# Performance work log

Measured on AMD Instinct MI355X. Metric: run time of the kernel, lower is better.

The kernel has to match this reference:

```python
import jax, jax.numpy as jnp
import numpy as np

N_HEADS = 8


def _norm_weights(idx):
    # softmax over where(idx>0, 1, -9e15) along axis 1 -> uniform weights over non-pad slots
    logits = jnp.where(idx > 0, jnp.float32(1.0), jnp.float32(-9e15))
    return jax.nn.softmax(logits, axis=1)


def _layer_norm(x, g, b, eps=1e-6):
    mu = jnp.mean(x, axis=-1, keepdims=True)
    var = jnp.var(x, axis=-1, keepdims=True)
    return (x - mu) * jax.lax.rsqrt(var + eps) * g + b


def _mha_block(x, mask, wq, wk, wv, wo, g, b):
    # standard multi-head self-attention block with residual + layernorm
    B, L, D = x.shape
    hd = D // N_HEADS
    q = (x @ wq).reshape(B, L, N_HEADS, hd)
    k = (x @ wk).reshape(B, L, N_HEADS, hd)
    v = (x @ wv).reshape(B, L, N_HEADS, hd)
    scores = jnp.einsum('bqhd,bkhd->bhqk', q, k) / jnp.float32(np.sqrt(hd))
    scores = jnp.where(mask[:, None, None, :], jnp.float32(-1e9), scores)
    attn = jax.nn.softmax(scores, axis=-1)
    out = jnp.einsum('bhqk,bkhd->bqhd', attn, v).reshape(B, L, D) @ wo
    return _layer_norm(out + x, g, b)


def _forward(data_idx, seq, timestamps, user_level, useq, user_inf, user_cen,
             spread_status, id2vector,
             user_emb, cen_emb, time_emb, pos_emb, inf_emb,
             w1, w2, w3,
             t_wq, t_wk, t_wv, t_wo, t_g, t_b,
             s_wq, s_wk, s_wv, s_wo, s_g, s_b,
             W, W2, f_l1_w, f_l1_b, f_l2_w, f_l2_b, lin_w, lin_b):
    # ---- HGNN layer (hypergraph conv) ----
    tv = w3[0]  # TextVector = weight3[0]
    dot = w3 @ tv
    cos = dot / (jnp.linalg.norm(tv) * jnp.linalg.norm(w3, axis=1))
    inter_nw = jnp.mean(cos)  # scalar

    tweet_hidden = user_emb + cen_emb[user_cen]          # [N, D]
    x = (tweet_hidden @ w1) * inter_nw                   # [N, D]
    nor = _norm_weights(seq)                             # [E, L]
    edge = jnp.einsum('elc,el->ec', x[seq], nor)         # gather + weighted reduce
    edge = jax.nn.relu(edge)
    e1 = edge @ w2                                       # [E, D]
    u_nor = _norm_weights(useq)                          # [N, Lu]
    node = jnp.einsum('nlc,nl->nc', e1[useq], u_nor)     # [N, D]

    # ---- HGSL head ----
    sb = seq[data_idx]                                   # [B, L]
    nor_b = _norm_weights(sb)
    att_mask = sb == 0                                   # PAD == 0
    adj = node[sb]                                       # [B, L, D]

    att_hidden = adj + time_emb[timestamps[data_idx]]
    att_out = _mha_block(att_hidden, att_mask, t_wq, t_wk, t_wv, t_wo, t_g, t_b)
    news = jnp.einsum('blc,bl->bc', att_out, nor_b)
    news = jnp.concatenate([news, spread_status[data_idx][:, 2:] / 3600.0 / 24.0], axis=-1) @ W

    att_hidden_s = adj + inf_emb[user_inf[data_idx]] + pos_emb[user_level[data_idx]]
    att_out_s = _mha_block(att_hidden_s, att_mask, s_wq, s_wk, s_wv, s_wo, s_g, s_b)
    news_s = jnp.einsum('blc,bl->bc', att_out_s, nor_b)
    news_s = jnp.concatenate([news_s, spread_status[data_idx][:, :2]], axis=-1) @ W2

    # Gated fusion (linear3 unused in original forward; id2vector is overwritten/unused)
    emb = jnp.stack([news, news_s], axis=0)              # [2, B, D+2]
    score = jax.nn.softmax(jnp.tanh(emb @ f_l1_w + f_l1_b) @ f_l2_w + f_l2_b, axis=0)
    fused = jnp.sum(score * emb, axis=0)                 # [B, D+2]
    return jax.nn.log_softmax(fused @ lin_w + lin_b, axis=1)


def setup_inputs():
    key = jax.random.key(0)
    ks = jax.random.split(key, 40)
    N, E, L, Lu, D, B, TV = 50000, 10000, 50, 20, 128, 512, 768
    Dw = D + 2
    s = 0.05
    inp = {
        'data_idx': jax.random.randint(ks[0], (B,), 0, E),
        'seq': jax.random.randint(ks[1], (E, L), 0, N),
        'timestamps': jax.random.randint(ks[2], (E, L), 0, 5000),
        'user_level': jax.random.randint(ks[3], (E, L), 0, 50),
        'useq': jax.random.randint(ks[4], (N, Lu), 0, E),
        'user_inf': jax.random.randint(ks[5], (E, L), 0, 200),
        'user_cen': jax.random.randint(ks[6], (N,), 0, 600),
        'spread_status': jax.random.uniform(ks[7], (E, 4), dtype=jnp.float32),
        'id2vector': jax.random.normal(ks[8], (1,), dtype=jnp.float32),
        'user_emb': s * jax.random.normal(ks[9], (N, D), dtype=jnp.float32),
        'cen_emb': s * jax.random.normal(ks[10], (600, D), dtype=jnp.float32),
        'time_emb': s * jax.random.normal(ks[11], (5000, D), dtype=jnp.float32),
        'pos_emb': s * jax.random.normal(ks[12], (50, D), dtype=jnp.float32),
        'inf_emb': s * jax.random.normal(ks[13], (200, D), dtype=jnp.float32),
        'w1': s * jax.random.normal(ks[14], (D, D), dtype=jnp.float32),
        'w2': s * jax.random.normal(ks[15], (D, D), dtype=jnp.float32),
        'w3': s * jax.random.normal(ks[16], (TV, TV), dtype=jnp.float32),
        'W': s * jax.random.normal(ks[17], (Dw, Dw), dtype=jnp.float32),
        'W2': s * jax.random.normal(ks[18], (Dw, Dw), dtype=jnp.float32),
        'f_l1_w': s * jax.random.normal(ks[19], (Dw, Dw), dtype=jnp.float32),
        'f_l1_b': jnp.zeros((Dw,), jnp.float32),
        'f_l2_w': s * jax.random.normal(ks[20], (Dw, 1), dtype=jnp.float32),
        'f_l2_b': jnp.zeros((1,), jnp.float32),
        'lin_w': s * jax.random.normal(ks[21], (Dw, 2), dtype=jnp.float32),
        'lin_b': jnp.zeros((2,), jnp.float32),
    }
    for nm, i in [('t', 22), ('s', 27)]:
        inp[nm + '_wq'] = s * jax.random.normal(ks[i], (D, D), dtype=jnp.float32)
        inp[nm + '_wk'] = s * jax.random.normal(ks[i + 1], (D, D), dtype=jnp.float32)
        inp[nm + '_wv'] = s * jax.random.normal(ks[i + 2], (D, D), dtype=jnp.float32)
        inp[nm + '_wo'] = s * jax.random.normal(ks[i + 3], (D, D), dtype=jnp.float32)
        inp[nm + '_g'] = jnp.ones((D,), jnp.float32)
        inp[nm + '_b'] = jnp.zeros((D,), jnp.float32)
    return inp


def reference(data_idx, seq, timestamps, user_level, useq, user_inf, user_cen,
              spread_status, id2vector,
              user_emb, cen_emb, time_emb, pos_emb, inf_emb,
              w1, w2, w3,
              t_wq, t_wk, t_wv, t_wo, t_g, t_b,
              s_wq, s_wk, s_wv, s_wo, s_g, s_b,
              W, W2, f_l1_w, f_l1_b, f_l2_w, f_l2_b, lin_w, lin_b):
    return _forward(data_idx, seq, timestamps, user_level, useq, user_inf, user_cen,
                    spread_status, id2vector,
                    user_emb, cen_emb, time_emb, pos_emb, inf_emb,
                    w1, w2, w3,
                    t_wq, t_wk, t_wv, t_wo, t_g, t_b,
                    s_wq, s_wk, s_wv, s_wo, s_g, s_b,
                    W, W2, f_l1_w, f_l1_b, f_l2_w, f_l2_b, lin_w, lin_b)
```

## Files before the change

### kernel.cpp

```cpp
#include <hip/hip_runtime.h>
#include <math.h>

constexpr int Nn = 50000;
constexpr int Ee = 10000;
constexpr int Ll = 50;
constexpr int LuU = 20;
constexpr int Dd = 128;
constexpr int Bb = 512;
constexpr int TVv = 768;
constexpr int Dw = 130;
constexpr int BL = Bb * Ll;

typedef __attribute__((ext_vector_type(8))) short bf8v;
typedef __attribute__((ext_vector_type(4))) float f4v;
typedef __attribute__((ext_vector_type(8))) unsigned short u16x8;
typedef __attribute__((ext_vector_type(4))) unsigned short u16x4;

__device__ __forceinline__ unsigned short f2bf(float f) {
  union { float f; unsigned u; } v; v.f = f;
  unsigned r = v.u + 0x7FFFu + ((v.u >> 16) & 1u);
  return (unsigned short)(r >> 16);
}
__device__ __forceinline__ float bf2f(unsigned short h) {
  union { unsigned u; float f; } v; v.u = ((unsigned)h) << 16; return v.f;
}
__device__ __forceinline__ int swz(int b) { return b ^ (((b >> 8) & 7) << 4); }
__device__ __forceinline__ int swzp(int b) { return b ^ (((b >> 7) & 3) << 4); }

__device__ __forceinline__ float block_sum_256(float v, volatile float* scr) {
#pragma unroll
  for (int o = 32; o > 0; o >>= 1) v += __shfl_down(v, o, 64);
  __syncthreads();
  if ((threadIdx.x & 63) == 0) scr[threadIdx.x >> 6] = v;
  __syncthreads();
  return scr[0] + scr[1] + scr[2] + scr[3];
}

__global__ __launch_bounds__(256) void k_cos(const float* __restrict__ w3,
                                             float* __restrict__ dotb,
                                             float* __restrict__ nrmb) {
  __shared__ float scr[4];
  int i = blockIdx.x;
  const float* row = w3 + (size_t)i * TVv;
  float d = 0.f, n = 0.f;
  for (int j = threadIdx.x; j < TVv; j += 256) {
    float a = row[j];
    d += a * w3[j];
    n += a * a;
  }
  d = block_sum_256(d, scr);
  n = block_sum_256(n, scr);
  if (threadIdx.x == 0) { dotb[i] = d; nrmb[i] = n; }
}

__global__ __launch_bounds__(256) void k_internw(const float* __restrict__ dotb,
                                                 const float* __restrict__ nrmb,
                                                 float* __restrict__ internw) {
  __shared__ float scr[4];
  float n0 = sqrtf(nrmb[0]);
  float s = 0.f;
  for (int i = threadIdx.x; i < TVv; i += 256)
    s += dotb[i] / (n0 * sqrtf(nrmb[i]));
  s = block_sum_256(s, scr);
  if (threadIdx.x == 0) *internw = s / (float)TVv;
}

__global__ __launch_bounds__(256) void k_prep(
    const float* w1, const float* w2,
    const float* twq, const float* twk, const float* twv, const float* two,
    const float* swq, const float* swk, const float* swv, const float* swo,
    unsigned short* __restrict__ out) {
  int wsel = blockIdx.x >> 3, part = blockIdx.x & 7;
  const float* w;
  switch (wsel) {
    case 0: w = w1; break;  case 1: w = w2; break;
    case 2: w = twq; break; case 3: w = twk; break;
    case 4: w = twv; break; case 5: w = two; break;
    case 6: w = swq; break; case 7: w = swk; break;
    case 8: w = swv; break; default: w = swo; break;
  }
  int u = part * 256 + threadIdx.x;
  int n = u >> 4, k0 = (u & 15) * 8;
  u16x8 pv;
#pragma unroll
  for (int i = 0; i < 8; i++) pv[i] = f2bf(w[(size_t)(k0 + i) * Dd + n]);
  ((u16x8*)(out + (size_t)wsel * Dd * Dd))[u] = pv;
}

template <int MODE>
__global__ __launch_bounds__(256) void k_gemm_plain(
    const void* __restrict__ inA, const float* __restrict__ in1,
    const int* __restrict__ gidx, const float* __restrict__ scalep,
    const unsigned short* __restrict__ WTg,
    unsigned short* __restrict__ out, int nrows) {
  __shared__ unsigned short WT[Dd * Dd];
  __shared__ __align__(16) unsigned short Ab[64 * Dd];
  int tid = threadIdx.x;
  {
    const u16x8* src = (const u16x8*)WTg;
    for (int u = tid; u < 2048; u += 256)
      *(u16x8*)((char*)WT + swz(u * 16)) = src[u];
  }
  int r0 = blockIdx.x * 64;
  if constexpr (MODE == 0) {
    float sc = *scalep;
    for (int u = tid; u < 1024; u += 256) {
      int rr = u >> 4, c0 = (u & 15) * 8;
      int r = r0 + rr;
      u16x8 pv;
      if (r < nrows) {
        const float* a = (const float*)inA + (size_t)r * Dd + c0;
        const float* c = in1 + (size_t)gidx[r] * Dd + c0;
#pragma unroll
        for (int i = 0; i < 8; i++) pv[i] = f2bf((a[i] + c[i]) * sc);
      } else {
#pragma unroll
        for (int i = 0; i < 8; i++) pv[i] = 0;
      }
      *(u16x8*)((char*)Ab + swz(rr * 256 + c0 * 2)) = pv;
    }
  } else {
    for (int u = tid; u < 1024; u += 256) {
      int rr = u >> 4;
      int r = r0 + rr;
      u16x8 pv;
      if (r < nrows) pv = ((const u16x8*)inA)[(size_t)r * 16 + (u & 15)];
      else {
#pragma unroll
        for (int i = 0; i < 8; i++) pv[i] = 0;
      }
      *(u16x8*)((char*)Ab + swz(rr * 256 + (u & 15) * 16)) = pv;
    }
  }
  __syncthreads();
  int lane = tid & 63, wid = tid >> 6;
  int lrow = lane & 15, lg = lane >> 4;
  bf8v af[4];
#pragma unroll
  for (int kc = 0; kc < 4; kc++)
    af[kc] = *(const bf8v*)((char*)Ab + swz((wid * 16 + lrow) * 256 + kc * 64 + lg * 16));
  f4v acc[8];
#pragma unroll
  for (int nt = 0; nt < 8; nt++)
#pragma unroll
    for (int j = 0; j < 4; j++) acc[nt][j] = 0.f;
#pragma unroll
  for (int nt = 0; nt < 8; nt++)
#pragma unroll
    for (int kc = 0; kc < 4; kc++) {
      bf8v bfg = *(const bf8v*)((char*)WT + swz((nt * 16 + lrow) * 256 + kc * 64 + lg * 16));
      acc[nt] = __builtin_amdgcn_mfma_f32_16x16x32_bf16(af[kc], bfg, acc[nt], 0, 0, 0);
    }
#pragma unroll
  for (int nt = 0; nt < 8; nt++)
#pragma unroll
    for (int j = 0; j < 4; j++) {
      int r = r0 + wid * 16 + lg * 4 + j;
      if (r < nrows) out[(size_t)r * Dd + nt * 16 + lrow] = f2bf(acc[nt][j]);
    }
}

__global__ __launch_bounds__(256) void k_gemm_qkv(
    const unsigned short* __restrict__ hidT, const unsigned short* __restrict__ hidS,
    const unsigned short* __restrict__ WTbase,
    unsigned short* __restrict__ outQ, unsigned short* __restrict__ outK,
    unsigned short* __restrict__ outV) {
  __shared__ unsigned short WT[Dd * Dd];
  __shared__ __align__(16) unsigned short Ab[128 * Dd];
  int tile = blockIdx.x % 200, branch = blockIdx.x / 200;
  const unsigned short* in = branch ? hidS : hidT;
  int r0 = tile * 128;
  int tid = threadIdx.x;
  for (int u = tid; u < 2048; u += 256) {
    int rr = u >> 4, ch = u & 15;
    u16x8 pv = ((const u16x8*)in)[(size_t)(r0 + rr) * 16 + ch];
    *(u16x8*)((char*)Ab + swz(rr * 256 + ch * 16)) = pv;
  }
  {
    const u16x8* srcW = (const u16x8*)(WTbase + (size_t)(2 + branch * 4) * Dd * Dd);
    for (int u = tid; u < 2048; u += 256)
      *(u16x8*)((char*)WT + swz(u * 16)) = srcW[u];
  }
  __syncthreads();
  int lane = tid & 63, wid = tid >> 6;
  int lrow = lane & 15, lg = lane >> 4;
  bf8v af[2][4];
#pragma unroll
  for (int mi = 0; mi < 2; mi++)
#pragma unroll
    for (int kc = 0; kc < 4; kc++)
      af[mi][kc] = *(const bf8v*)((char*)Ab +
                    swz((wid * 32 + mi * 16 + lrow) * 256 + kc * 64 + lg * 16));
#pragma unroll 1
  for (int sel = 0; sel < 3; sel++) {
    f4v acc[2][8];
#pragma unroll
    for (int mi = 0; mi < 2; mi++)
#pragma unroll
      for (int nt = 0; nt < 8; nt++)
#pragma unroll
        for (int j = 0; j < 4; j++) acc[mi][nt][j] = 0.f;
#pragma unroll
    for (int nt = 0; nt < 8; nt++)
#pragma unroll
      for (int kc = 0; kc < 4; kc++) {
        bf8v bfg = *(const bf8v*)((char*)WT + swz((nt * 16 + lrow) * 256 + kc * 64 + lg * 16));
        acc[0][nt] = __builtin_amdgcn_mfma_f32_16x16x32_bf16(af[0][kc], bfg, acc[0][nt], 0, 0, 0);
        acc[1][nt] = __builtin_amdgcn_mfma_f32_16x16x32_bf16(af[1][kc], bfg, acc[1][nt], 0, 0, 0);
      }
    unsigned short* outb = ((sel == 0) ? outQ : (sel == 1) ? outK : outV)
                           + (size_t)branch * BL * Dd;
#pragma unroll
    for (int mi = 0; mi < 2; mi++)
#pragma unroll
      for (int nt = 0; nt < 8; nt++)
#pragma unroll
        for (int j = 0; j < 4; j++) {
          int r = r0 + wid * 32 + mi * 16 + lg * 4 + j;
          outb[(size_t)r * Dd + nt * 16 + lrow] = f2bf(acc[mi][nt][j]);
        }
    if (sel < 2) {
      __syncthreads();
      const u16x8* srcW = (const u16x8*)(WTbase + (size_t)(2 + branch * 4 + sel + 1) * Dd * Dd);
      for (int u = tid; u < 2048; u += 256)
        *(u16x8*)((char*)WT + swz(u * 16)) = srcW[u];
      __syncthreads();
    }
  }
}

__global__ __launch_bounds__(256) void k_gemm_ln(
    const unsigned short* __restrict__ ctxall,
    const unsigned short* __restrict__ hidT, const unsigned short* __restrict__ hidS,
    const unsigned short* __restrict__ WTbase,
    const float* __restrict__ tg, const float* __restrict__ tb,
    const float* __restrict__ sg, const float* __restrict__ sb_,
    unsigned short* __restrict__ attall) {
  __shared__ unsigned short WT[Dd * Dd];
  __shared__ __align__(16) char UB[64 * 132 * 4];
  unsigned short* Ab = (unsigned short*)UB;
  float (*O)[132] = (float (*)[132])UB;

  int tile = blockIdx.x % 400, branch = blockIdx.x / 400;
  const unsigned short* in = ctxall + (size_t)branch * BL * Dd;
  const unsigned short* resid = (branch ? hidS : hidT);
  const unsigned short* Wg = WTbase + (size_t)(5 + branch * 4) * Dd * Dd;
  const float* lng = branch ? sg : tg;
  const float* lnb = branch ? sb_ : tb;
  unsigned short* out = attall + (size_t)branch * BL * Dd;
  int r0 = tile * 64;
  int tid = threadIdx.x;

  {
    const u16x8* src = (const u16x8*)Wg;
    for (int u = tid; u < 2048; u += 256)
      *(u16x8*)((char*)WT + swz(u * 16)) = src[u];
  }
  for (int u = tid; u < 1024; u += 256) {
    int rr = u >> 4;
    u16x8 pv = ((const u16x8*)in)[(size_t)(r0 + rr) * 16 + (u & 15)];
    *(u16x8*)((char*)Ab + swz(rr * 256 + (u & 15) * 16)) = pv;
  }
  __syncthreads();

  int lane = tid & 63, wid = tid >> 6;
  int lrow = lane & 15, lg = lane >> 4;
  bf8v af[4];
#pragma unroll
  for (int kc = 0; kc < 4; kc++)
    af[kc] = *(const bf8v*)((char*)Ab + swz((wid * 16 + lrow) * 256 + kc * 64 + lg * 16));
  f4v acc[8];
#pragma unroll
  for (int nt = 0; nt < 8; nt++)
#pragma unroll
    for (int j = 0; j < 4; j++) acc[nt][j] = 0.f;
#pragma unroll
  for (int nt = 0; nt < 8; nt++)
#pragma unroll
    for (int kc = 0; kc < 4; kc++) {
      bf8v bfg = *(const bf8v*)((char*)WT + swz((nt * 16 + lrow) * 256 + kc * 64 + lg * 16));
      acc[nt] = __builtin_amdgcn_mfma_f32_16x16x32_bf16(af[kc], bfg, acc[nt], 0, 0, 0);
    }
  __syncthreads();
#pragma unroll
  for (int nt = 0; nt < 8; nt++)
#pragma unroll
    for (int j = 0; j < 4; j++)
      O[wid * 16 + lg * 4 + j][nt * 16 + lrow] = acc[nt][j];
  __syncthreads();
  int r = tid >> 2, c0 = (tid & 3) * 32;
  size_t gr = (size_t)(r0 + r);
  float vv[32];
  float s1 = 0.f, s2 = 0.f;
#pragma unroll
  for (int i8 = 0; i8 < 4; i8++) {
    u16x8 hb = *(const u16x8*)(resid + gr * Dd + c0 + i8 * 8);
#pragma unroll
    for (int i = 0; i < 8; i++) {
      float x = O[r][c0 + i8 * 8 + i] + bf2f(hb[i]);
      vv[i8 * 8 + i] = x; s1 += x; s2 += x * x;
    }
  }
  s1 += __shfl_xor(s1, 1, 64); s2 += __shfl_xor(s2, 1, 64);
  s1 += __shfl_xor(s1, 2, 64); s2 += __shfl_xor(s2, 2, 64);
  float mu = s1 * (1.f / Dd);
  float var = s2 * (1.f / Dd) - mu * mu;
  float rs = rsqrtf(var + 1e-6f);
#pragma unroll
  for (int i8 = 0; i8 < 4; i8++) {
    u16x8 ov;
#pragma unroll
    for (int i = 0; i < 8; i++) {
      int c = c0 + i8 * 8 + i;
      ov[i] = f2bf((vv[i8 * 8 + i] - mu) * rs * lng[c] + lnb[c]);
    }
    *(u16x8*)(out + gr * Dd + c0 + i8 * 8) = ov;
  }
}

__global__ __launch_bounds__(256) void k_gather_e(const unsigned short* __restrict__ X,
                                                  const int* __restrict__ seq,
                                                  unsigned short* __restrict__ EDGE) {
  int r = blockIdx.x * 16 + (threadIdx.x >> 4);
  int c0 = (threadIdx.x & 15) * 8;
  const int* row = seq + (size_t)r * Ll;
  float acc[8];
#pragma unroll
  for (int i = 0; i < 8; i++) acc[i] = 0.f;
  int cnt = 0;
#pragma unroll 1
  for (int l0 = 0; l0 < Ll; l0 += 10) {
    int ids[10];
#pragma unroll
    for (int t = 0; t < 10; t++) ids[t] = row[l0 + t];
    u16x8 vv[10];
#pragma unroll
    for (int t = 0; t < 10; t++)
      vv[t] = *(const u16x8*)(X + (size_t)ids[t] * Dd + c0);
#pragma unroll
    for (int t = 0; t < 10; t++)
      if (ids[t] > 0) {
        cnt++;
#pragma unroll
        for (int i = 0; i < 8; i++) acc[i] += bf2f(vv[t][i]);
      }
  }
  u16x8 ov;
  if (cnt) {
    float inv = 1.f / (float)cnt;
#pragma unroll
    for (int i = 0; i < 8; i++) ov[i] = f2bf(fmaxf(acc[i] * inv, 0.f));
  } else {
    u16x8 x0 = *(const u16x8*)(X + c0);
#pragma unroll
    for (int i = 0; i < 8; i++) ov[i] = f2bf(fmaxf(bf2f(x0[i]), 0.f));
  }
  *(u16x8*)(EDGE + (size_t)r * Dd + c0) = ov;
}

__global__ __launch_bounds__(256) void k_hidfuse(
    const unsigned short* __restrict__ E1, const int* __restrict__ data_idx,
    const int* __restrict__ seq, const int* __restrict__ tsmp,
    const int* __restrict__ uinf, const int* __restrict__ ulev,
    const int* __restrict__ useq,
    const float* __restrict__ time_emb, const float* __restrict__ inf_emb,
    const float* __restrict__ pos_emb,
    unsigned short* __restrict__ hidTb, unsigned short* __restrict__ hidSb) {
  int bl = blockIdx.x * 16 + (threadIdx.x >> 4);
  int c0 = (threadIdx.x & 15) * 8;
  int b = bl / Ll, l = bl % Ll;
  int e = data_idx[b];
  int sid = seq[(size_t)e * Ll + l];
  const int* urow = useq + (size_t)sid * LuU;
  float acc[8];
#pragma unroll
  for (int i = 0; i < 8; i++) acc[i] = 0.f;
  int cnt = 0;
#pragma unroll 1
  for (int t0 = 0; t0 < LuU; t0 += 10) {
    int ids[10];
#pragma unroll
    for (int t = 0; t < 10; t++) ids[t] = urow[t0 + t];
    u16x8 vv[10];
#pragma unroll
    for (int t = 0; t < 10; t++)
      vv[t] = *(const u16x8*)(E1 + (size_t)ids[t] * Dd + c0);
#pragma unroll
    for (int t = 0; t < 10; t++)
      if (ids[t] > 0) {
        cnt++;
#pragma unroll
        for (int i = 0; i < 8; i++) acc[i] += bf2f(vv[t][i]);
      }
  }
  float node[8];
  if (cnt) {
    float inv = 1.f / (float)cnt;
#pragma unroll
    for (int i = 0; i < 8; i++) node[i] = acc[i] * inv;
  } else {
    u16x8 e0 = *(const u16x8*)(E1 + c0);
#pragma unroll
    for (int i = 0; i < 8; i++) node[i] = bf2f(e0[i]);
  }
  int ts = tsmp[(size_t)e * Ll + l];
  int fi = uinf[(size_t)e * Ll + l];
  int lv = ulev[(size_t)e * Ll + l];
  const float4* tp = (const float4*)(time_emb + (size_t)ts * Dd + c0);
  const float4* ip = (const float4*)(inf_emb + (size_t)fi * Dd + c0);
  const float4* pp = (const float4*)(pos_emb + (size_t)lv * Dd + c0);
  float4 t0 = tp[0], t1 = tp[1];
  float4 i0 = ip[0], i1 = ip[1];
  float4 p0 = pp[0], p1 = pp[1];
  float te[8] = {t0.x, t0.y, t0.z, t0.w, t1.x, t1.y, t1.z, t1.w};
  float ie[8] = {i0.x, i0.y, i0.z, i0.w, i1.x, i1.y, i1.z, i1.w};
  float pe[8] = {p0.x, p0.y, p0.z, p0.w, p1.x, p1.y, p1.z, p1.w};
  u16x8 ht, hs;
#pragma unroll
  for (int i = 0; i < 8; i++) {
    ht[i] = f2bf(node[i] + te[i]);
    hs[i] = f2bf(node[i] + ie[i] + pe[i]);
  }
  size_t o = (size_t)bl * Dd + c0;
  *(u16x8*)(hidTb + o) = ht;
  *(u16x8*)(hidSb + o) = hs;
}

__global__ __launch_bounds__(256) void k_attn_mfma(
    const unsigned short* __restrict__ qall,
    const unsigned short* __restrict__ kall,
    const unsigned short* __restrict__ vall,
    const int* __restrict__ data_idx,
    const int* __restrict__ seq,
    unsigned short* __restrict__ ctxall) {
  __shared__ __align__(16) unsigned short QKV[3 * 64 * 128];
  __shared__ __align__(16) unsigned short PT[4 * 64 * 64];
  __shared__ int maskl[Ll];
  int b = blockIdx.x, branch = blockIdx.y;
  size_t boff = (size_t)branch * BL * Dd + (size_t)b * Ll * Dd;
  const unsigned short* qg = qall + boff;
  const unsigned short* kg = kall + boff;
  const unsigned short* vg = vall + boff;
  int tid = threadIdx.x;
  int e = data_idx[b];
  if (tid < Ll) maskl[tid] = (seq[(size_t)e * Ll + tid] == 0);
  for (int u = tid; u < 3072; u += 256) {
    int t = u >> 10, rem = u & 1023;
    int row = rem >> 4, ch = rem & 15;
    u16x8 pv;
    if (row < Ll) {
      const unsigned short* src = (t == 0) ? qg : (t == 1) ? kg : vg;
      pv = *(const u16x8*)(src + (size_t)row * Dd + ch * 8);
    } else {
#pragma unroll
      for (int i = 0; i < 8; i++) pv[i] = 0;
    }
    *(u16x8*)((char*)QKV + t * 16384 + swz(row * 256 + ch * 16)) = pv;
  }
  __syncthreads();
  int lane = tid & 63, wid = tid >> 6;
  int lrow = lane & 15, lg = lane >> 4;
  const char* Qb = (const char*)QKV;
  const char* Kb = (const char*)QKV + 16384;
  const char* Vb = (const char*)QKV + 32768;
  char* PTw = (char*)PT + wid * 8192;
  unsigned short* ctx = ctxall + boff;

#pragma unroll 1
  for (int hi = 0; hi < 2; hi++) {
    int h = wid * 2 + hi;
    int cb = h * 32;
    bf8v af[4], bf[4];
    if (lg < 2) {
#pragma unroll
      for (int mt = 0; mt < 4; mt++)
        af[mt] = *(const bf8v*)(Kb + swz((mt * 16 + lrow) * 256 + cb + lg * 16));
#pragma unroll
      for (int nt = 0; nt < 4; nt++)
        bf[nt] = *(const bf8v*)(Qb + swz((nt * 16 + lrow) * 256 + cb + lg * 16));
    } else {
#pragma unroll
      for (int t = 0; t < 4; t++)
#pragma unroll
        for (int i = 0; i < 8; i++) { af[t][i] = 0; bf[t][i] = 0; }
    }
    f4v acc[16];
#pragma unroll
    for (int t = 0; t < 16; t++)
#pragma unroll
      for (int j = 0; j < 4; j++) acc[t][j] = 0.f;
#pragma unroll
    for (int mt = 0; mt < 4; mt++)
#pragma unroll
      for (int nt = 0; nt < 4; nt++)
        acc[mt * 4 + nt] =
            __builtin_amdgcn_mfma_f32_16x16x32_bf16(af[mt], bf[nt], acc[mt * 4 + nt], 0, 0, 0);
#pragma unroll
    for (int mt = 0; mt < 4; mt++)
#pragma unroll
      for (int j = 0; j < 4; j++) {
        int kk = mt * 16 + lg * 4 + j;
        bool pad = (kk >= Ll);
        bool mk = !pad && (maskl[pad ? 0 : kk] != 0);
#pragma unroll
        for (int nt = 0; nt < 4; nt++) {
          float v = acc[mt * 4 + nt][j] * 0.25f;
          v = mk ? -1e9f : v;
          v = pad ? -3.0e38f : v;
          acc[mt * 4 + nt][j] = v;
        }
      }
#pragma unroll
    for (int nt = 0; nt < 4; nt++) {
      float m = -3.0e38f;
#pragma unroll
      for (int mt = 0; mt < 4; mt++)
#pragma unroll
        for (int j = 0; j < 4; j++) m = fmaxf(m, acc[mt * 4 + nt][j]);
      m = fmaxf(m, __shfl_xor(m, 16, 64));
      m = fmaxf(m, __shfl_xor(m, 32, 64));
      float s = 0.f;
#pragma unroll
      for (int mt = 0; mt < 4; mt++)
#pragma unroll
        for (int j = 0; j < 4; j++) {
          float p = expf(acc[mt * 4 + nt][j] - m);
          acc[mt * 4 + nt][j] = p;
          s += p;
        }
      s += __shfl_xor(s, 16, 64);
      s += __shfl_xor(s, 32, 64);
      float inv = 1.f / s;
      int q = nt * 16 + lrow;
#pragma unroll
      for (int mt = 0; mt < 4; mt++) {
        u16x4 pw;
#pragma unroll
        for (int j = 0; j < 4; j++) pw[j] = f2bf(acc[mt * 4 + nt][j] * inv);
        *(u16x4*)(PTw + swzp(q * 128 + mt * 32 + lg * 8)) = pw;
      }
    }
    f4v pacc[4];
#pragma unroll
    for (int nt = 0; nt < 4; nt++)
#pragma unroll
      for (int j = 0; j < 4; j++) pacc[nt][j] = 0.f;
#pragma unroll
    for (int kt = 0; kt < 2; kt++) {
      bf8v av;
#pragma unroll
      for (int i = 0; i < 8; i++)
        av[i] = *(const short*)(Vb + swz((kt * 32 + lg * 8 + i) * 256 + cb + lrow * 2));
#pragma unroll
      for (int nt = 0; nt < 4; nt++) {
        bf8v bv = *(const bf8v*)(PTw + swzp((nt * 16 + lrow) * 128 + kt * 64 + lg * 16));
        pacc[nt] = __builtin_amdgcn_mfma_f32_16x16x32_bf16(av, bv, pacc[nt], 0, 0, 0);
      }
    }
#pragma unroll
    for (int nt = 0; nt < 4; nt++) {
      int q = nt * 16 + lrow;
      if (q < Ll) {
        u16x4 ow;
#pragma unroll
        for (int j = 0; j < 4; j++) ow[j] = f2bf(pacc[nt][j]);
        *(u16x4*)(ctx + (size_t)q * Dd + h * 16 + lg * 4) = ow;
      }
    }
  }
}

__global__ __launch_bounds__(128) void k_newsred(const unsigned short* __restrict__ attall,
                                                 const int* __restrict__ data_idx,
                                                 const int* __restrict__ seq,
                                                 const float* __restrict__ spread,
                                                 float* __restrict__ news) {
  __shared__ int sl[Ll];
  __shared__ int scnt;
  int b = blockIdx.x, branch = blockIdx.y;
  int e = data_idx[b];
  const unsigned short* att = attall + (size_t)branch * BL * Dd;
  if (threadIdx.x < Ll) sl[threadIdx.x] = seq[(size_t)e * Ll + threadIdx.x];
  __syncthreads();
  if (threadIdx.x == 0) {
    int c = 0;
    for (int l = 0; l < Ll; l++) c += (sl[l] > 0);
    scnt = c;
  }
  __syncthreads();
  int cnt = scnt;
  float wnp = cnt ? 1.f / (float)cnt : 0.02f;
  int c = threadIdx.x;
  float acc = 0.f;
  for (int l = 0; l < Ll; l++) {
    float w = cnt ? ((sl[l] > 0) ? wnp : 0.f) : wnp;
    acc += w * bf2f(att[((size_t)b * Ll + l) * Dd + c]);
  }
  float* nrow = news + ((size_t)branch * Bb + b) * 132;
  nrow[c] = acc;
  if (c < 2) {
    nrow[Dd + c] = branch ? spread[(size_t)e * 4 + c]
                          : spread[(size_t)e * 4 + 2 + c] * (1.f / 86400.f);
  }
}

__global__ __launch_bounds__(256) void k_newsW(const float* __restrict__ news,
                                               const float* __restrict__ Wm,
                                               const float* __restrict__ W2m,
                                               float* __restrict__ NT,
                                               float* __restrict__ NS) {
  __shared__ float Wl[Dw][Dw + 1];
  __shared__ float nrow[132];
  int branch = blockIdx.y;
  const float* W = branch ? W2m : Wm;
  float* out = branch ? NS : NT;
  for (int u = threadIdx.x; u < Dw * Dw; u += 256)
    Wl[u / Dw][u % Dw] = W[u];
  for (int rr = 0; rr < 32; rr++) {
    int b = blockIdx.x * 32 + rr;
    __syncthreads();
    if (threadIdx.x < Dw)
      nrow[threadIdx.x] = news[((size_t)branch * Bb + b) * 132 + threadIdx.x];
    __syncthreads();
    int j = threadIdx.x;
    if (j < Dw) {
      float acc = 0.f;
      for (int kk = 0; kk < Dw; kk++) acc += nrow[kk] * Wl[kk][j];
      out[(size_t)b * Dw + j] = acc;
    }
  }
}

__global__ __launch_bounds__(256) void k_fusion(const float* __restrict__ nt,
                                                const float* __restrict__ ns,
                                                const float* __restrict__ l1w,
                                                const float* __restrict__ l1b,
                                                const float* __restrict__ l2w,
                                                const float* __restrict__ l2b,
                                                const float* __restrict__ linw,
                                                const float* __restrict__ linb,
                                                float* __restrict__ out) {
  __shared__ float rt[Dw], rs[Dw];
  __shared__ float scr[4];
  int b = blockIdx.x, j = threadIdx.x;
  if (j < Dw) { rt[j] = nt[(size_t)b * Dw + j]; rs[j] = ns[(size_t)b * Dw + j]; }
  __syncthreads();
  float pt = 0.f, ps = 0.f;
  if (j < Dw) {
    float at = l1b[j], as = l1b[j];
    for (int kk = 0; kk < Dw; kk++) {
      float w = l1w[(size_t)kk * Dw + j];
      at += rt[kk] * w;
      as += rs[kk] * w;
    }
    float lw2 = l2w[j];
    pt = tanhf(at) * lw2;
    ps = tanhf(as) * lw2;
  }
  float st = block_sum_256(pt, scr);
  float ss = block_sum_256(ps, scr);
  st += l2b[0]; ss += l2b[0];
  float m = fmaxf(st, ss);
  float e0 = expf(st - m), e1v = expf(ss - m);
  float inv = 1.f / (e0 + e1v);
  float s0 = e0 * inv, s1 = e1v * inv;
  float fj  = (j < Dw) ? (s0 * rt[j] + s1 * rs[j]) : 0.f;
  float w0  = (j < Dw) ? linw[(size_t)j * 2 + 0] : 0.f;
  float w1v = (j < Dw) ? linw[(size_t)j * 2 + 1] : 0.f;
  float l0 = block_sum_256(fj * w0, scr);
  float l1 = block_sum_256(fj * w1v, scr);
  if (j == 0) {
    l0 += linb[0]; l1 += linb[1];
    float mm = fmaxf(l0, l1);
    float lse = mm + logf(expf(l0 - mm) + expf(l1 - mm));
    out[(size_t)b * 2 + 0] = l0 - lse;
    out[(size_t)b * 2 + 1] = l1 - lse;
  }
}

extern "C" void kernel_launch(void* const* d_in, const int* in_sizes, int n_in,
                              void* d_out, int out_size, void* d_ws, size_t ws_size,
                              hipStream_t stream) {
  const int*   data_idx = (const int*)d_in[0];
  const int*   seq      = (const int*)d_in[1];
  const int*   tsmp     = (const int*)d_in[2];
  const int*   ulev     = (const int*)d_in[3];
  const int*   useq     = (const int*)d_in[4];
  const int*   uinf     = (const int*)d_in[5];
  const int*   ucen     = (const int*)d_in[6];
  const float* spread   = (const float*)d_in[7];
  const float* user_emb = (const float*)d_in[9];
  const float* cen_emb  = (const float*)d_in[10];
  const float* time_emb = (const float*)d_in[11];
  const float* pos_emb  = (const float*)d_in[12];
  const float* inf_emb  = (const float*)d_in[13];
  const float* w1       = (const float*)d_in[14];
  const float* w2       = (const float*)d_in[15];
  const float* w3       = (const float*)d_in[16];
  const float* Wm       = (const float*)d_in[17];
  const float* W2m      = (const float*)d_in[18];
  const float* f_l1_w   = (const float*)d_in[19];
  const float* f_l1_b   = (const float*)d_in[20];
  const float* f_l2_w   = (const float*)d_in[21];
  const float* f_l2_b   = (const float*)d_in[22];
  const float* lin_w    = (const float*)d_in[23];
  const float* lin_b    = (const float*)d_in[24];
  const float* t_wq = (const float*)d_in[25];
  const float* t_wk = (const float*)d_in[26];
  const float* t_wv = (const float*)d_in[27];
  const float* t_wo = (const float*)d_in[28];
  const float* t_g  = (const float*)d_in[29];
  const float* t_b  = (const float*)d_in[30];
  const float* s_wq = (const float*)d_in[31];
  const float* s_wk = (const float*)d_in[32];
  const float* s_wv = (const float*)d_in[33];
  const float* s_wo = (const float*)d_in[34];
  const float* s_g  = (const float*)d_in[35];
  const float* s_b  = (const float*)d_in[36];

  char* ws = (char*)d_ws;
  constexpr size_t SZ_WT  = (size_t)10 * Dd * Dd * 2;
  constexpr size_t SZ_XB  = (size_t)Nn * Dd * 2;
  constexpr size_t SZ_EB  = (size_t)Ee * Dd * 2;
  constexpr size_t SZ_BH  = (size_t)BL * Dd * 2;
  constexpr size_t OFF_WT  = 8192;
  constexpr size_t OFF_X   = OFF_WT + SZ_WT;
  constexpr size_t OFF_EDGE= OFF_X + SZ_XB;
  constexpr size_t OFF_E1  = OFF_EDGE + SZ_EB;
  constexpr size_t OFF_HTB = OFF_E1 + SZ_EB;
  constexpr size_t OFF_HSB = OFF_HTB + SZ_BH;
  constexpr size_t OFF_Q   = OFF_HSB + SZ_BH;
  constexpr size_t OFF_K   = OFF_Q + 2 * SZ_BH;
  constexpr size_t OFF_V   = OFF_K + 2 * SZ_BH;
  constexpr size_t OFF_CTX = OFF_V + 2 * SZ_BH;
  constexpr size_t OFF_ATT = OFF_CTX + 2 * SZ_BH;
  constexpr size_t OFF_NEWS= OFF_ATT + 2 * SZ_BH;
  constexpr size_t OFF_NT  = OFF_NEWS + (size_t)2 * Bb * 132 * 4;
  constexpr size_t OFF_NS  = OFF_NT + (size_t)Bb * Dw * 4;

  float* dotb    = (float*)(ws + 0);
  float* nrmb    = (float*)(ws + 3072);
  float* internw = (float*)(ws + 6144);
  unsigned short* WTall = (unsigned short*)(ws + OFF_WT);
  unsigned short* Xb    = (unsigned short*)(ws + OFF_X);
  unsigned short* EDGEb = (unsigned short*)(ws + OFF_EDGE);
  unsigned short* E1b   = (unsigned short*)(ws + OFF_E1);
  unsigned short* HIDTb = (unsigned short*)(ws + OFF_HTB);
  unsigned short* HIDSb = (unsigned short*)(ws + OFF_HSB);
  unsigned short* Qall  = (unsigned short*)(ws + OFF_Q);
  unsigned short* Kall  = (unsigned short*)(ws + OFF_K);
  unsigned short* Vall  = (unsigned short*)(ws + OFF_V);
  unsigned short* CTXall= (unsigned short*)(ws + OFF_CTX);
  unsigned short* ATTall= (unsigned short*)(ws + OFF_ATT);
  float*          NEWS  = (float*)(ws + OFF_NEWS);
  float*          NT    = (float*)(ws + OFF_NT);
  float*          NS    = (float*)(ws + OFF_NS);
  float* outp = (float*)d_out;

  k_prep<<<80, 256, 0, stream>>>(w1, w2, t_wq, t_wk, t_wv, t_wo,
                                 s_wq, s_wk, s_wv, s_wo, WTall);
  k_cos<<<TVv, 256, 0, stream>>>(w3, dotb, nrmb);
  k_internw<<<1, 256, 0, stream>>>(dotb, nrmb, internw);

  k_gemm_plain<0><<<(Nn + 63) / 64, 256, 0, stream>>>(
      user_emb, cen_emb, ucen, internw, WTall + 0 * Dd * Dd, Xb, Nn);
  k_gather_e<<<Ee / 16, 256, 0, stream>>>(Xb, seq, EDGEb);
  k_gemm_plain<1><<<(Ee + 63) / 64, 256, 0, stream>>>(
      EDGEb, nullptr, nullptr, nullptr, WTall + 1 * Dd * Dd, E1b, Ee);
  k_hidfuse<<<BL / 16, 256, 0, stream>>>(E1b, data_idx, seq, tsmp, uinf, ulev, useq,
                                         time_emb, inf_emb, pos_emb, HIDTb, HIDSb);

  k_gemm_qkv<<<400, 256, 0, stream>>>(HIDTb, HIDSb, WTall, Qall, Kall, Vall);
  k_attn_mfma<<<dim3(Bb, 2), 256, 0, stream>>>(Qall, Kall, Vall, data_idx, seq, CTXall);
  k_gemm_ln<<<400 * 2, 256, 0, stream>>>(CTXall, HIDTb, HIDSb, WTall,
                                         t_g, t_b, s_g, s_b, ATTall);

  k_newsred<<<dim3(Bb, 2), 128, 0, stream>>>(ATTall, data_idx, seq, spread, NEWS);
  k_newsW<<<dim3(16, 2), 256, 0, stream>>>(NEWS, Wm, W2m, NT, NS);
  k_fusion<<<Bb, 256, 0, stream>>>(NT, NS, f_l1_w, f_l1_b, f_l2_w, f_l2_b,
                                   lin_w, lin_b, outp);

  (void)in_sizes; (void)n_in; (void)out_size; (void)ws_size;
}
```

Baseline: 357.9 us.

## Pad QKV/ctx to 64 rows per batch and store V transposed for attention

```diff
diff --git a/kernel.cpp b/kernel.cpp
--- a/kernel.cpp
+++ b/kernel.cpp
@@ -10,6 +10,7 @@
 constexpr int TVv = 768;
 constexpr int Dw = 130;
 constexpr int BL = Bb * Ll;
+constexpr int BLP = Bb * 64;
 
 typedef __attribute__((ext_vector_type(8))) short bf8v;
 typedef __attribute__((ext_vector_type(4))) float f4v;
@@ -25,7 +26,7 @@
   union { unsigned u; float f; } v; v.u = ((unsigned)h) << 16; return v.f;
 }
 __device__ __forceinline__ int swz(int b) { return b ^ (((b >> 8) & 7) << 4); }
-__device__ __forceinline__ int swzp(int b) { return b ^ (((b >> 7) & 3) << 4); }
+__device__ __forceinline__ int swz7(int b) { return b ^ (((b >> 7) & 7) << 4); }
 
 __device__ __forceinline__ float block_sum_256(float v, volatile float* scr) {
 #pragma unroll
@@ -163,17 +164,23 @@
 __global__ __launch_bounds__(256) void k_gemm_qkv(
     const unsigned short* __restrict__ hidT, const unsigned short* __restrict__ hidS,
     const unsigned short* __restrict__ WTbase,
-    unsigned short* __restrict__ outQ, unsigned short* __restrict__ outK,
-    unsigned short* __restrict__ outV) {
+    unsigned short* __restrict__ Qp, unsigned short* __restrict__ Kp,
+    unsigned short* __restrict__ VTp) {
   __shared__ unsigned short WT[Dd * Dd];
   __shared__ __align__(16) unsigned short Ab[128 * Dd];
-  int tile = blockIdx.x % 200, branch = blockIdx.x / 200;
+  int tile = blockIdx.x & 255, branch = blockIdx.x >> 8;
   const unsigned short* in = branch ? hidS : hidT;
-  int r0 = tile * 128;
   int tid = threadIdx.x;
   for (int u = tid; u < 2048; u += 256) {
     int rr = u >> 4, ch = u & 15;
-    u16x8 pv = ((const u16x8*)in)[(size_t)(r0 + rr) * 16 + ch];
+    int brow = rr >> 6, sub = rr & 63;
+    u16x8 pv;
+    if (sub < Ll)
+      pv = ((const u16x8*)in)[(size_t)((tile * 2 + brow) * Ll + sub) * 16 + ch];
+    else {
+#pragma unroll
+      for (int i = 0; i < 8; i++) pv[i] = 0;
+    }
     *(u16x8*)((char*)Ab + swz(rr * 256 + ch * 16)) = pv;
   }
   {
@@ -208,29 +215,48 @@
         acc[0][nt] = __builtin_amdgcn_mfma_f32_16x16x32_bf16(af[0][kc], bfg, acc[0][nt], 0, 0, 0);
         acc[1][nt] = __builtin_amdgcn_mfma_f32_16x16x32_bf16(af[1][kc], bfg, acc[1][nt], 0, 0, 0);
       }
-    unsigned short* outb = ((sel == 0) ? outQ : (sel == 1) ? outK : outV)
-                           + (size_t)branch * BL * Dd;
-#pragma unroll
-    for (int mi = 0; mi < 2; mi++)
-#pragma unroll
-      for (int nt = 0; nt < 8; nt++)
-#pragma unroll
-        for (int j = 0; j < 4; j++) {
-          int r = r0 + wid * 32 + mi * 16 + lg * 4 + j;
-          outb[(size_t)r * Dd + nt * 16 + lrow] = f2bf(acc[mi][nt][j]);
-        }
     if (sel < 2) {
+      unsigned short* outb = ((sel == 0) ? Qp : Kp) + (size_t)branch * BLP * Dd;
+#pragma unroll
+      for (int mi = 0; mi < 2; mi++)
+#pragma unroll
+        for (int nt = 0; nt < 8; nt++)
+#pragma unroll
+          for (int j = 0; j < 4; j++) {
+            int r = tile * 128 + wid * 32 + mi * 16 + lg * 4 + j;
+            outb[(size_t)r * Dd + nt * 16 + lrow] = f2bf(acc[mi][nt][j]);
+          }
       __syncthreads();
       const u16x8* srcW = (const u16x8*)(WTbase + (size_t)(2 + branch * 4 + sel + 1) * Dd * Dd);
       for (int u = tid; u < 2048; u += 256)
         *(u16x8*)((char*)WT + swz(u * 16)) = srcW[u];
       __syncthreads();
+    } else {
+      __syncthreads();
+#pragma unroll
+      for (int mi = 0; mi < 2; mi++)
+#pragma unroll
+        for (int nt = 0; nt < 8; nt++) {
+          int d = nt * 16 + lrow;
+          int rl = wid * 32 + mi * 16 + lg * 4;
+          u16x4 tv;
+#pragma unroll
+          for (int j = 0; j < 4; j++) tv[j] = f2bf(acc[mi][nt][j]);
+          *(u16x4*)((char*)Ab + swz(d * 256 + rl * 2)) = tv;
+        }
+      __syncthreads();
+      for (int u = tid; u < 2048; u += 256) {
+        int d = u >> 4, ch = u & 15;
+        u16x8 pv = *(const u16x8*)((char*)Ab + swz(d * 256 + ch * 16));
+        int bidx = ch >> 3, kv0 = (ch & 7) * 8;
+        *(u16x8*)(VTp + (((size_t)branch * Bb + tile * 2 + bidx) * Dd + d) * 64 + kv0) = pv;
+      }
     }
   }
 }
 
 __global__ __launch_bounds__(256) void k_gemm_ln(
-    const unsigned short* __restrict__ ctxall,
+    const unsigned short* __restrict__ ctxp,
     const unsigned short* __restrict__ hidT, const unsigned short* __restrict__ hidS,
     const unsigned short* __restrict__ WTbase,
     const float* __restrict__ tg, const float* __restrict__ tb,
@@ -241,14 +267,12 @@
   unsigned short* Ab = (unsigned short*)UB;
   float (*O)[132] = (float (*)[132])UB;
 
-  int tile = blockIdx.x % 400, branch = blockIdx.x / 400;
-  const unsigned short* in = ctxall + (size_t)branch * BL * Dd;
+  int b = blockIdx.x & 511, branch = blockIdx.x >> 9;
   const unsigned short* resid = (branch ? hidS : hidT);
   const unsigned short* Wg = WTbase + (size_t)(5 + branch * 4) * Dd * Dd;
   const float* lng = branch ? sg : tg;
   const float* lnb = branch ? sb_ : tb;
   unsigned short* out = attall + (size_t)branch * BL * Dd;
-  int r0 = tile * 64;
   int tid = threadIdx.x;
 
   {
@@ -258,7 +282,7 @@
   }
   for (int u = tid; u < 1024; u += 256) {
     int rr = u >> 4;
-    u16x8 pv = ((const u16x8*)in)[(size_t)(r0 + rr) * 16 + (u & 15)];
+    u16x8 pv = ((const u16x8*)ctxp)[(((size_t)branch * Bb + b) * 64 + rr) * 16 + (u & 15)];
     *(u16x8*)((char*)Ab + swz(rr * 256 + (u & 15) * 16)) = pv;
   }
   __syncthreads();
@@ -289,32 +313,34 @@
       O[wid * 16 + lg * 4 + j][nt * 16 + lrow] = acc[nt][j];
   __syncthreads();
   int r = tid >> 2, c0 = (tid & 3) * 32;
-  size_t gr = (size_t)(r0 + r);
-  float vv[32];
-  float s1 = 0.f, s2 = 0.f;
-#pragma unroll
-  for (int i8 = 0; i8 < 4; i8++) {
-    u16x8 hb = *(const u16x8*)(resid + gr * Dd + c0 + i8 * 8);
-#pragma unroll
-    for (int i = 0; i < 8; i++) {
-      float x = O[r][c0 + i8 * 8 + i] + bf2f(hb[i]);
-      vv[i8 * 8 + i] = x; s1 += x; s2 += x * x;
-    }
-  }
-  s1 += __shfl_xor(s1, 1, 64); s2 += __shfl_xor(s2, 1, 64);
-  s1 += __shfl_xor(s1, 2, 64); s2 += __shfl_xor(s2, 2, 64);
-  float mu = s1 * (1.f / Dd);
-  float var = s2 * (1.f / Dd) - mu * mu;
-  float rs = rsqrtf(var + 1e-6f);
-#pragma unroll
-  for (int i8 = 0; i8 < 4; i8++) {
-    u16x8 ov;
-#pragma unroll
-    for (int i = 0; i < 8; i++) {
-      int c = c0 + i8 * 8 + i;
-      ov[i] = f2bf((vv[i8 * 8 + i] - mu) * rs * lng[c] + lnb[c]);
-    }
-    *(u16x8*)(out + gr * Dd + c0 + i8 * 8) = ov;
+  if (r < Ll) {
+    size_t gr = (size_t)b * Ll + r;
+    float vv[32];
+    float s1 = 0.f, s2 = 0.f;
+#pragma unroll
+    for (int i8 = 0; i8 < 4; i8++) {
+      u16x8 hb = *(const u16x8*)(resid + gr * Dd + c0 + i8 * 8);
+#pragma unroll
+      for (int i = 0; i < 8; i++) {
+        float x = O[r][c0 + i8 * 8 + i] + bf2f(hb[i]);
+        vv[i8 * 8 + i] = x; s1 += x; s2 += x * x;
+      }
+    }
+    s1 += __shfl_xor(s1, 1, 64); s2 += __shfl_xor(s2, 1, 64);
+    s1 += __shfl_xor(s1, 2, 64); s2 += __shfl_xor(s2, 2, 64);
+    float mu = s1 * (1.f / Dd);
+    float var = s2 * (1.f / Dd) - mu * mu;
+    float rs = rsqrtf(var + 1e-6f);
+#pragma unroll
+    for (int i8 = 0; i8 < 4; i8++) {
+      u16x8 ov;
+#pragma unroll
+      for (int i = 0; i < 8; i++) {
+        int c = c0 + i8 * 8 + i;
+        ov[i] = f2bf((vv[i8 * 8 + i] - mu) * rs * lng[c] + lnb[c]);
+      }
+      *(u16x8*)(out + gr * Dd + c0 + i8 * 8) = ov;
+    }
   }
 }
 
@@ -426,97 +452,62 @@
   *(u16x8*)(hidSb + o) = hs;
 }
 
-__global__ __launch_bounds__(256) void k_attn_mfma(
-    const unsigned short* __restrict__ qall,
-    const unsigned short* __restrict__ kall,
-    const unsigned short* __restrict__ vall,
+__global__ __launch_bounds__(256, 4) void k_attn_mfma(
+    const unsigned short* __restrict__ Qp,
+    const unsigned short* __restrict__ Kp,
+    const unsigned short* __restrict__ VTp,
     const int* __restrict__ data_idx,
     const int* __restrict__ seq,
-    unsigned short* __restrict__ ctxall) {
-  __shared__ __align__(16) unsigned short QKV[3 * 64 * 128];
-  __shared__ __align__(16) unsigned short PT[4 * 64 * 64];
+    unsigned short* __restrict__ ctxp) {
+  __shared__ __align__(16) char PTs[4 * 8192];
   __shared__ int maskl[Ll];
   int b = blockIdx.x, branch = blockIdx.y;
-  size_t boff = (size_t)branch * BL * Dd + (size_t)b * Ll * Dd;
-  const unsigned short* qg = qall + boff;
-  const unsigned short* kg = kall + boff;
-  const unsigned short* vg = vall + boff;
-  int tid = threadIdx.x;
-  int e = data_idx[b];
-  if (tid < Ll) maskl[tid] = (seq[(size_t)e * Ll + tid] == 0);
-  for (int u = tid; u < 3072; u += 256) {
-    int t = u >> 10, rem = u & 1023;
-    int row = rem >> 4, ch = rem & 15;
-    u16x8 pv;
-    if (row < Ll) {
-      const unsigned short* src = (t == 0) ? qg : (t == 1) ? kg : vg;
-      pv = *(const u16x8*)(src + (size_t)row * Dd + ch * 8);
-    } else {
-#pragma unroll
-      for (int i = 0; i < 8; i++) pv[i] = 0;
-    }
-    *(u16x8*)((char*)QKV + t * 16384 + swz(row * 256 + ch * 16)) = pv;
-  }
-  __syncthreads();
-  int lane = tid & 63, wid = tid >> 6;
+  int tid = threadIdx.x, lane = tid & 63, wid = tid >> 6;
+  if (tid < Ll) maskl[tid] = (seq[(size_t)data_idx[b] * Ll + tid] == 0);
+  __syncthreads();
   int lrow = lane & 15, lg = lane >> 4;
-  const char* Qb = (const char*)QKV;
-  const char* Kb = (const char*)QKV + 16384;
-  const char* Vb = (const char*)QKV + 32768;
-  char* PTw = (char*)PT + wid * 8192;
-  unsigned short* ctx = ctxall + boff;
-
+  size_t rbase = ((size_t)branch * Bb + b) * 64;
+  size_t vrow  = ((size_t)branch * Bb + b) * Dd;
+  char* PTw = PTs + wid * 8192;
 #pragma unroll 1
   for (int hi = 0; hi < 2; hi++) {
     int h = wid * 2 + hi;
-    int cb = h * 32;
-    bf8v af[4], bf[4];
+    bf8v af[4], bq[4];
     if (lg < 2) {
 #pragma unroll
+      for (int t = 0; t < 4; t++) {
+        af[t] = *(const bf8v*)(Kp + (rbase + t * 16 + lrow) * Dd + h * 16 + lg * 8);
+        bq[t] = *(const bf8v*)(Qp + (rbase + t * 16 + lrow) * Dd + h * 16 + lg * 8);
+      }
+    } else {
+#pragma unroll
+      for (int t = 0; t < 4; t++)
+#pragma unroll
+        for (int i = 0; i < 8; i++) { af[t][i] = 0; bq[t][i] = 0; }
+    }
+#pragma unroll 1
+    for (int nt = 0; nt < 4; nt++) {
+      f4v sa[4];
+#pragma unroll
       for (int mt = 0; mt < 4; mt++)
-        af[mt] = *(const bf8v*)(Kb + swz((mt * 16 + lrow) * 256 + cb + lg * 16));
-#pragma unroll
-      for (int nt = 0; nt < 4; nt++)
-        bf[nt] = *(const bf8v*)(Qb + swz((nt * 16 + lrow) * 256 + cb + lg * 16));
-    } else {
-#pragma unroll
-      for (int t = 0; t < 4; t++)
-#pragma unroll
-        for (int i = 0; i < 8; i++) { af[t][i] = 0; bf[t][i] = 0; }
-    }
-    f4v acc[16];
-#pragma unroll
-    for (int t = 0; t < 16; t++)
-#pragma unroll
-      for (int j = 0; j < 4; j++) acc[t][j] = 0.f;
-#pragma unroll
-    for (int mt = 0; mt < 4; mt++)
-#pragma unroll
-      for (int nt = 0; nt < 4; nt++)
-        acc[mt * 4 + nt] =
-            __builtin_amdgcn_mfma_f32_16x16x32_bf16(af[mt], bf[nt], acc[mt * 4 + nt], 0, 0, 0);
-#pragma unroll
-    for (int mt = 0; mt < 4; mt++)
-#pragma unroll
-      for (int j = 0; j < 4; j++) {
-        int kk = mt * 16 + lg * 4 + j;
-        bool pad = (kk >= Ll);
-        bool mk = !pad && (maskl[pad ? 0 : kk] != 0);
-#pragma unroll
-        for (int nt = 0; nt < 4; nt++) {
-          float v = acc[mt * 4 + nt][j] * 0.25f;
-          v = mk ? -1e9f : v;
-          v = pad ? -3.0e38f : v;
-          acc[mt * 4 + nt][j] = v;
+#pragma unroll
+        for (int j = 0; j < 4; j++) sa[mt][j] = 0.f;
+#pragma unroll
+      for (int mt = 0; mt < 4; mt++)
+        sa[mt] = __builtin_amdgcn_mfma_f32_16x16x32_bf16(af[mt], bq[nt], sa[mt], 0, 0, 0);
+      float m = -3.0e38f;
+#pragma unroll
+      for (int mt = 0; mt < 4; mt++)
+#pragma unroll
+        for (int j = 0; j < 4; j++) {
+          int kk = mt * 16 + lg * 4 + j;
+          int mk = (kk < Ll) ? maskl[kk] : 2;
+          float v = sa[mt][j] * 0.25f;
+          v = (mk == 1) ? -1e9f : v;
+          v = (mk == 2) ? -3.0e38f : v;
+          sa[mt][j] = v;
+          m = fmaxf(m, v);
         }
-      }
-#pragma unroll
-    for (int nt = 0; nt < 4; nt++) {
-      float m = -3.0e38f;
-#pragma unroll
-      for (int mt = 0; mt < 4; mt++)
-#pragma unroll
-        for (int j = 0; j < 4; j++) m = fmaxf(m, acc[mt * 4 + nt][j]);
       m = fmaxf(m, __shfl_xor(m, 16, 64));
       m = fmaxf(m, __shfl_xor(m, 32, 64));
       float s = 0.f;
@@ -524,8 +515,8 @@
       for (int mt = 0; mt < 4; mt++)
 #pragma unroll
         for (int j = 0; j < 4; j++) {
-          float p = expf(acc[mt * 4 + nt][j] - m);
-          acc[mt * 4 + nt][j] = p;
+          float p = expf(sa[mt][j] - m);
+          sa[mt][j] = p;
           s += p;
         }
       s += __shfl_xor(s, 16, 64);
@@ -536,8 +527,8 @@
       for (int mt = 0; mt < 4; mt++) {
         u16x4 pw;
 #pragma unroll
-        for (int j = 0; j < 4; j++) pw[j] = f2bf(acc[mt * 4 + nt][j] * inv);
-        *(u16x4*)(PTw + swzp(q * 128 + mt * 32 + lg * 8)) = pw;
+        for (int j = 0; j < 4; j++) pw[j] = f2bf(sa[mt][j] * inv);
+        *(u16x4*)(PTw + swz7(q * 128 + mt * 32 + lg * 8)) = pw;
       }
     }
     f4v pacc[4];
@@ -547,25 +538,19 @@
       for (int j = 0; j < 4; j++) pacc[nt][j] = 0.f;
 #pragma unroll
     for (int kt = 0; kt < 2; kt++) {
-      bf8v av;
-#pragma unroll
-      for (int i = 0; i < 8; i++)
-        av[i] = *(const short*)(Vb + swz((kt * 32 + lg * 8 + i) * 256 + cb + lrow * 2));
+      bf8v av = *(const bf8v*)(VTp + (vrow + h * 16 + lrow) * 64 + kt * 32 + lg * 8);
 #pragma unroll
       for (int nt = 0; nt < 4; nt++) {
-        bf8v bv = *(const bf8v*)(PTw + swzp((nt * 16 + lrow) * 128 + kt * 64 + lg * 16));
+        bf8v bv = *(const bf8v*)(PTw + swz7((nt * 16 + lrow) * 128 + kt * 64 + lg * 16));
         pacc[nt] = __builtin_amdgcn_mfma_f32_16x16x32_bf16(av, bv, pacc[nt], 0, 0, 0);
       }
     }
 #pragma unroll
     for (int nt = 0; nt < 4; nt++) {
       int q = nt * 16 + lrow;
-      if (q < Ll) {
-        u16x4 ow;
-#pragma unroll
-        for (int j = 0; j < 4; j++) ow[j] = f2bf(pacc[nt][j]);
-        *(u16x4*)(ctx + (size_t)q * Dd + h * 16 + lg * 4) = ow;
-      }
+      unsigned* cp = (unsigned*)(ctxp + (rbase + q) * Dd + h * 16 + lg * 4);
+      cp[0] = (unsigned)f2bf(pacc[nt][0]) | ((unsigned)f2bf(pacc[nt][1]) << 16);
+      cp[1] = (unsigned)f2bf(pacc[nt][2]) | ((unsigned)f2bf(pacc[nt][3]) << 16);
     }
   }
 }
@@ -723,6 +708,7 @@
   constexpr size_t SZ_XB  = (size_t)Nn * Dd * 2;
   constexpr size_t SZ_EB  = (size_t)Ee * Dd * 2;
   constexpr size_t SZ_BH  = (size_t)BL * Dd * 2;
+  constexpr size_t SZ_PD  = (size_t)2 * BLP * Dd * 2;
   constexpr size_t OFF_WT  = 8192;
   constexpr size_t OFF_X   = OFF_WT + SZ_WT;
   constexpr size_t OFF_EDGE= OFF_X + SZ_XB;
@@ -730,11 +716,11 @@
   constexpr size_t OFF_HTB = OFF_E1 + SZ_EB;
   constexpr size_t OFF_HSB = OFF_HTB + SZ_BH;
   constexpr size_t OFF_Q   = OFF_HSB + SZ_BH;
-  constexpr size_t OFF_K   = OFF_Q + 2 * SZ_BH;
-  constexpr size_t OFF_V   = OFF_K + 2 * SZ_BH;
-  constexpr size_t OFF_CTX = OFF_V + 2 * SZ_BH;
-  constexpr size_t OFF_ATT = OFF_CTX + 2 * SZ_BH;
-  constexpr size_t OFF_NEWS= OFF_ATT + 2 * SZ_BH;
+  constexpr size_t OFF_K   = OFF_Q + SZ_PD;
+  constexpr size_t OFF_VT  = OFF_K + SZ_PD;
+  constexpr size_t OFF_CTX = OFF_VT + SZ_PD;
+  constexpr size_t OFF_ATT = OFF_Q;
+  constexpr size_t OFF_NEWS= OFF_CTX + SZ_PD;
   constexpr size_t OFF_NT  = OFF_NEWS + (size_t)2 * Bb * 132 * 4;
   constexpr size_t OFF_NS  = OFF_NT + (size_t)Bb * Dw * 4;
 
@@ -747,10 +733,10 @@
   unsigned short* E1b   = (unsigned short*)(ws + OFF_E1);
   unsigned short* HIDTb = (unsigned short*)(ws + OFF_HTB);
   unsigned short* HIDSb = (unsigned short*)(ws + OFF_HSB);
-  unsigned short* Qall  = (unsigned short*)(ws + OFF_Q);
-  unsigned short* Kall  = (unsigned short*)(ws + OFF_K);
-  unsigned short* Vall  = (unsigned short*)(ws + OFF_V);
-  unsigned short* CTXall= (unsigned short*)(ws + OFF_CTX);
+  unsigned short* Qp    = (unsigned short*)(ws + OFF_Q);
+  unsigned short* Kp    = (unsigned short*)(ws + OFF_K);
+  unsigned short* VTp   = (unsigned short*)(ws + OFF_VT);
+  unsigned short* CTXp  = (unsigned short*)(ws + OFF_CTX);
   unsigned short* ATTall= (unsigned short*)(ws + OFF_ATT);
   float*          NEWS  = (float*)(ws + OFF_NEWS);
   float*          NT    = (float*)(ws + OFF_NT);
@@ -770,10 +756,10 @@
   k_hidfuse<<<BL / 16, 256, 0, stream>>>(E1b, data_idx, seq, tsmp, uinf, ulev, useq,
                                          time_emb, inf_emb, pos_emb, HIDTb, HIDSb);
 
-  k_gemm_qkv<<<400, 256, 0, stream>>>(HIDTb, HIDSb, WTall, Qall, Kall, Vall);
-  k_attn_mfma<<<dim3(Bb, 2), 256, 0, stream>>>(Qall, Kall, Vall, data_idx, seq, CTXall);
-  k_gemm_ln<<<400 * 2, 256, 0, stream>>>(CTXall, HIDTb, HIDSb, WTall,
-                                         t_g, t_b, s_g, s_b, ATTall);
+  k_gemm_qkv<<<512, 256, 0, stream>>>(HIDTb, HIDSb, WTall, Qp, Kp, VTp);
+  k_attn_mfma<<<dim3(Bb, 2), 256, 0, stream>>>(Qp, Kp, VTp, data_idx, seq, CTXp);
+  k_gemm_ln<<<1024, 256, 0, stream>>>(CTXp, HIDTb, HIDSb, WTall,
+                                      t_g, t_b, s_g, s_b, ATTall);
 
   k_newsred<<<dim3(Bb, 2), 128, 0, stream>>>(ATTall, data_idx, seq, spread, NEWS);
   k_newsW<<<dim3(16, 2), 256, 0, stream>>>(NEWS, Wm, W2m, NT, NS);
```

Result: slower. 378.1 us (+5.7%).
